# Performance work log

Measured on AMD Instinct MI355X. Metric: run time of the kernel, lower is better.

The kernel has to match this reference:

```python
import jax, jax.numpy as jnp
import numpy as np

B, S, D = 4, 2048, 1024


def setup_inputs() -> dict:
    key = jax.random.key(0)
    k1, k2, k3, k4, k5 = jax.random.split(key, 5)
    x = jax.random.normal(k1, (B, S, D), dtype=jnp.float32)
    mask = jax.random.randint(k2, (B, S), 0, 2).astype(jnp.bool_)
    # glorot-uniform-like init as keras add_weight default
    lim = float(np.sqrt(6.0 / (D + D)))
    q_w = jax.random.uniform(k3, (D, D), minval=-lim, maxval=lim, dtype=jnp.float32)
    k_w = jax.random.uniform(k4, (D, D), minval=-lim, maxval=lim, dtype=jnp.float32)
    v_w = jax.random.uniform(k5, (D, D), minval=-lim, maxval=lim, dtype=jnp.float32)
    return {"x": x, "mask": mask, "q_w": q_w, "k_w": k_w, "v_w": v_w}


def reference(x, mask, q_w, k_w, v_w):
    scale = 1.0 / jnp.sqrt(jnp.asarray(x.shape[-1], dtype=x.dtype))
    q = jnp.einsum('bsi,ij->bsj', x, q_w)
    k = jnp.einsum('bsi,ij->bsj', x, k_w)
    y = jnp.einsum('bsi,bzi->bsz', q, k) * scale  # [B,S,S] scores
    # additive mask applied along the query axis, exactly as the source
    m = (~mask).astype(x.dtype)[:, :, None]
    y = y + m * (-1e9)
    v = jnp.einsum('bsi,ij->bsj', x, v_w)
    p = jax.nn.softmax(y, axis=-1)
    return jnp.einsum('bsz,bzi->bsi', p, v)
```

## Files before the change

kernel.cpp:

```cpp
#include <hip/hip_runtime.h>
#include <hip/hip_bf16.h>

typedef __attribute__((ext_vector_type(8))) short short8;
typedef __attribute__((ext_vector_type(4))) float floatx4;

struct ushort4v { unsigned short x, y, z, w; };

static __device__ __forceinline__ unsigned short f2bf(float f) {
    __hip_bfloat16 h = __float2bfloat16(f);
    return *reinterpret_cast<unsigned short*>(&h);
}

static __device__ __forceinline__ float bf2f(unsigned short u) {
    unsigned int v = ((unsigned int)u) << 16;
    return *reinterpret_cast<float*>(&v);
}

#define ASYNC_COPY16(gsrc, ldst)                                                            \
    __builtin_amdgcn_global_load_lds((const __attribute__((address_space(1))) void*)(gsrc), \
                                     (__attribute__((address_space(3))) void*)(ldst), 16, 0, 0)

static __device__ __forceinline__ void block_barrier() {
    asm volatile("" ::: "memory");
    __builtin_amdgcn_s_barrier();
    asm volatile("" ::: "memory");
}

__global__ void mask_detect(const unsigned char* __restrict__ m, int* __restrict__ flag) {
    __shared__ int s_or;
    if (threadIdx.x == 0) s_or = 0;
    __syncthreads();
    int acc = 0;
    for (int i = threadIdx.x; i < 8192; i += 256)
        if (i & 3) acc |= m[i];
    atomicOr(&s_or, acc);
    __syncthreads();
    if (threadIdx.x == 0) *flag = (s_or != 0) ? 1 : 0;
}

__global__ void mask_expand(const void* __restrict__ m, const int* __restrict__ flag,
                            float* __restrict__ keep, int n) {
    int i = blockIdx.x * 256 + threadIdx.x;
    if (i >= n) return;
    bool on;
    if (*flag)
        on = ((const unsigned char*)m)[i] != 0;
    else
        on = ((const int*)m)[i] != 0;
    keep[i] = on ? 1.0f : 0.0f;
}

__global__ __launch_bounds__(256) void convert_f32_bf16(const float* __restrict__ in,
                                                        unsigned short* __restrict__ out, long n4) {
    long i = (long)blockIdx.x * 256 + threadIdx.x;
    if (i >= n4) return;
    float4 v = ((const float4*)in)[i];
    ushort4v o;
    o.x = f2bf(v.x); o.y = f2bf(v.y); o.z = f2bf(v.z); o.w = f2bf(v.w);
    ((ushort4v*)out)[i] = o;
}

__global__ void transpose_w_kernel(const float* __restrict__ w0, const float* __restrict__ w1,
                                   const float* __restrict__ w2, unsigned short* __restrict__ out) {
    __shared__ float t[32][33];
    const float* w = blockIdx.z == 0 ? w0 : (blockIdx.z == 1 ? w1 : w2);
    unsigned short* o = out + (long)blockIdx.z * 1024 * 1024;
    int c0 = blockIdx.x * 32, r0 = blockIdx.y * 32;
    for (int i = threadIdx.y; i < 32; i += 8)
        t[i][threadIdx.x] = w[(long)(r0 + i) * 1024 + c0 + threadIdx.x];
    __syncthreads();
    for (int i = threadIdx.y; i < 32; i += 8)
        o[(long)(c0 + i) * 1024 + r0 + threadIdx.x] = f2bf(t[threadIdx.x][i]);
}

__global__ void transpose_bf16(const unsigned short* __restrict__ in, unsigned short* __restrict__ out,
                               int rows, int cols, long sIn, long sOut) {
    __shared__ unsigned short t[32][34];
    const unsigned short* ib = in + (long)blockIdx.z * sIn;
    unsigned short* ob = out + (long)blockIdx.z * sOut;
    int c0 = blockIdx.x * 32, r0 = blockIdx.y * 32;
    for (int i = threadIdx.y; i < 32; i += 8)
        t[i][threadIdx.x] = ib[(long)(r0 + i) * cols + c0 + threadIdx.x];
    __syncthreads();
    for (int i = threadIdx.y; i < 32; i += 8)
        ob[(long)(c0 + i) * rows + r0 + threadIdx.x] = t[threadIdx.x][i];
}

template <int EPI>
static __device__ __forceinline__ void gemm8_body(const unsigned short* __restrict__ A,
                                                  const unsigned short* __restrict__ B,
                                                  void* __restrict__ Cv,
                                                  const float* __restrict__ aux,
                                                  int K, int lda, int ldb, int ldc,
                                                  long sA, long sB, long sC, long sAux,
                                                  float scale) {
    constexpr int TILE = (128 + 256) * 32 * 2;
    __shared__ char sm[3 * TILE];

    const int tid = threadIdx.x;
    const int wid = tid >> 6, lane = tid & 63;
    const int wm  = wid >> 2, wn = wid & 3;
    const int fr  = lane & 15, fk = lane >> 4;
    const long m0 = (long)blockIdx.x * 128;
    const long n0 = (long)blockIdx.y * 256;
    const unsigned short* Ab = A + (long)blockIdx.z * sA + m0 * lda;
    const unsigned short* Bb = B + (long)blockIdx.z * sB + n0 * ldb;
    const int NT = K >> 5;

    floatx4 acc[4][4] = {};

    auto stage = [&](int kt, int buf) {
        char* dA = sm + buf * TILE;
        char* dB = dA + 128 * 64;
        const int kb = kt << 5;
        {
            int lam = tid * 16;
            int lg  = lam ^ (((lam >> 7) & 3) << 4);
            ASYNC_COPY16(Ab + (long)(lg >> 6) * lda + kb + ((lg & 63) >> 1), dA + lam);
        }
#pragma unroll
        for (int i = 0; i < 2; i++) {
            int lam = i * 8192 + tid * 16;
            int lg  = lam ^ (((lam >> 7) & 3) << 4);
            ASYNC_COPY16(Bb + (long)(lg >> 6) * ldb + kb + ((lg & 63) >> 1), dB + lam);
        }
    };

    stage(0, 0);
    stage(1, 1);

    int cur = 0;
    for (int t = 0; t < NT; t++) {
        if (t + 1 < NT) asm volatile("s_waitcnt vmcnt(3)" ::: "memory");
        else            asm volatile("s_waitcnt vmcnt(0)" ::: "memory");
        block_barrier();

        const char* bA = sm + cur * TILE;
        const char* bB = bA + 128 * 64;
        short8 af[4], bf[4];
#pragma unroll
        for (int mi = 0; mi < 4; mi++) {
            int row = wm * 64 + mi * 16 + fr;
            int c   = (fk * 16) ^ (((row >> 1) & 3) << 4);
            af[mi] = *(const short8*)(bA + row * 64 + c);
        }
#pragma unroll
        for (int ni = 0; ni < 4; ni++) {
            int row = wn * 64 + ni * 16 + fr;
            int c   = (fk * 16) ^ (((row >> 1) & 3) << 4);
            bf[ni] = *(const short8*)(bB + row * 64 + c);
        }
        if (t + 2 < NT) stage(t + 2, (cur + 2) % 3);

        __builtin_amdgcn_s_setprio(1);
#pragma unroll
        for (int mi = 0; mi < 4; mi++)
#pragma unroll
            for (int ni = 0; ni < 4; ni++)
                acc[mi][ni] = __builtin_amdgcn_mfma_f32_16x16x32_bf16(af[mi], bf[ni], acc[mi][ni], 0, 0, 0);
        __builtin_amdgcn_s_setprio(0);
        cur = (cur == 2) ? 0 : cur + 1;
    }

    const int crow = (lane >> 4) * 4;
    const int ccol = lane & 15;
#pragma unroll
    for (int mi = 0; mi < 4; mi++) {
#pragma unroll
        for (int j = 0; j < 4; j++) {
            long r = m0 + wm * 64 + mi * 16 + crow + j;
            float rowf = 0.0f;
            if (EPI == 1) rowf = scale * aux[(long)blockIdx.z * sAux + r];
            if (EPI == 2) rowf = aux[(long)blockIdx.z * sAux + r];
#pragma unroll
            for (int ni = 0; ni < 4; ni++) {
                long c = n0 + wn * 64 + ni * 16 + ccol;
                float v = acc[mi][ni][j];
                if (EPI == 0) {
                    ((unsigned short*)Cv)[(long)blockIdx.z * sC + r * ldc + c] = f2bf(v);
                } else if (EPI == 1) {
                    ((unsigned short*)Cv)[(long)blockIdx.z * sC + r * ldc + c] = f2bf(__expf(v * rowf));
                } else {
                    ((float*)Cv)[(long)blockIdx.z * sC + r * ldc + c] = v * rowf;
                }
            }
        }
    }
}

__global__ __launch_bounds__(512, 4) void gemm8_qkv(const unsigned short* __restrict__ A,
                                                    const unsigned short* __restrict__ B,
                                                    void* __restrict__ Cv,
                                                    int K, int lda, int ldb, int ldc,
                                                    long sA, long sB, long sC) {
    gemm8_body<0>(A, B, Cv, nullptr, K, lda, ldb, ldc, sA, sB, sC, 0L, 1.0f);
}

__global__ __launch_bounds__(512, 4) void gemm8_scores(const unsigned short* __restrict__ A,
                                                       const unsigned short* __restrict__ B,
                                                       void* __restrict__ Cv,
                                                       const float* __restrict__ keep,
                                                       int K, int lda, int ldb, int ldc,
                                                       long sA, long sB, long sC, long sAux,
                                                       float scale) {
    gemm8_body<1>(A, B, Cv, keep, K, lda, ldb, ldc, sA, sB, sC, sAux, scale);
}

__global__ __launch_bounds__(512, 4) void gemm8_pv(const unsigned short* __restrict__ A,
                                                   const unsigned short* __restrict__ B,
                                                   void* __restrict__ Cv,
                                                   const float* __restrict__ invsum,
                                                   int K, int lda, int ldb, int ldc,
                                                   long sA, long sB, long sC, long sAux) {
    gemm8_body<2>(A, B, Cv, invsum, K, lda, ldb, ldc, sA, sB, sC, sAux, 1.0f);
}

__global__ __launch_bounds__(256) void rowsum_inv(const unsigned short* __restrict__ P,
                                                  float* __restrict__ inv, long strideP) {
    const int tid = threadIdx.x;
    const long row = blockIdx.x;
    short8 v = ((const short8*)(P + row * strideP))[tid];
    float s = 0.0f;
#pragma unroll
    for (int i = 0; i < 8; i++) s += bf2f((unsigned short)v[i]);
#pragma unroll
    for (int i = 1; i < 64; i <<= 1) s += __shfl_xor(s, i);
    __shared__ float ss[4];
    if ((tid & 63) == 0) ss[tid >> 6] = s;
    __syncthreads();
    if (tid == 0) {
        float t = (ss[0] + ss[1]) + (ss[2] + ss[3]);
        inv[row] = 1.0f / t;
    }
}

extern "C" void kernel_launch(void* const* d_in, const int* in_sizes, int n_in,
                              void* d_out, int out_size, void* d_ws, size_t ws_size,
                              hipStream_t stream) {
    const float* x  = (const float*)d_in[0];
    const void*  mask = d_in[1];
    const float* qw = (const float*)d_in[2];
    const float* kw = (const float*)d_in[3];
    const float* vw = (const float*)d_in[4];
    float* out = (float*)d_out;

    constexpr int B = 4, S = 2048, D = 1024;
    constexpr long BS  = (long)B * S;
    constexpr long BSD = BS * D;

    char* w = (char*)d_ws;
    auto alloc = [&](size_t bytes) {
        char* p = w;
        w += (bytes + 255) & ~(size_t)255;
        return p;
    };
    int*            flag    = (int*)alloc(256);
    float*          keep    = (float*)alloc(BS * 4);
    float*          invsum  = (float*)alloc(BS * 4);
    unsigned short* xb      = (unsigned short*)alloc((size_t)BSD * 2);
    unsigned short* wT      = (unsigned short*)alloc((size_t)3 * D * D * 2);
    unsigned short* qkv     = (unsigned short*)alloc((size_t)3 * BSD * 2);
    unsigned short* Qb = qkv;
    unsigned short* Kb = qkv + BSD;
    unsigned short* Vb = qkv + 2 * BSD;
    unsigned short* Vt      = (unsigned short*)alloc((size_t)BSD * 2);

    size_t base_used = (size_t)(w - (char*)d_ws);
    size_t pB = (size_t)B * S * S * 2;
    bool batched = ws_size >= base_used + pB + 1024;

    unsigned short* P;
    if (batched) {
        P = (unsigned short*)alloc(pB);
    } else {
        P = (unsigned short*)alloc((size_t)S * S * 2);
    }

    const float scale = 0.03125f;

    mask_detect<<<1, 256, 0, stream>>>((const unsigned char*)mask, flag);
    mask_expand<<<(int)(BS / 256), 256, 0, stream>>>(mask, flag, keep, (int)BS);
    convert_f32_bf16<<<(int)(BSD / 1024), 256, 0, stream>>>(x, xb, BSD / 4);
    transpose_w_kernel<<<dim3(32, 32, 3), dim3(32, 8), 0, stream>>>(qw, kw, vw, wT);

    gemm8_qkv<<<dim3(64, 4, 3), 512, 0, stream>>>(xb, wT, qkv,
                                                  1024, 1024, 1024, 1024,
                                                  0L, (long)D * D, BSD);

    transpose_bf16<<<dim3(D / 32, S / 32, B), dim3(32, 8), 0, stream>>>(Vb, Vt, S, D,
                                                                        (long)S * D, (long)S * D);

    if (batched) {
        gemm8_scores<<<dim3(16, 8, B), 512, 0, stream>>>(Qb, Kb, P, keep,
                                                         1024, 1024, 1024, 2048,
                                                         (long)S * D, (long)S * D, (long)S * S, (long)S, scale);
        rowsum_inv<<<(int)BS, 256, 0, stream>>>(P, invsum, 2048);
        gemm8_pv<<<dim3(16, 4, B), 512, 0, stream>>>(P, Vt, out, invsum,
                                                     2048, 2048, 2048, 1024,
                                                     (long)S * S, (long)D * S, (long)S * D, (long)S);
    } else {
        for (int b = 0; b < B; b++) {
            gemm8_scores<<<dim3(16, 8, 1), 512, 0, stream>>>(Qb + (long)b * S * D, Kb + (long)b * S * D,
                                                             P, keep + (long)b * S,
                                                             1024, 1024, 1024, 2048,
                                                             0L, 0L, 0L, 0L, scale);
            rowsum_inv<<<S, 256, 0, stream>>>(P, invsum + (long)b * S, 2048);
            gemm8_pv<<<dim3(16, 4, 1), 512, 0, stream>>>(P, Vt + (long)b * D * S, out + (long)b * S * D,
                                                         invsum + (long)b * S,
                                                         2048, 2048, 2048, 1024,
                                                         0L, 0L, 0L, 0L);
        }
    }
}
```

Measured before the change: 178.6 us.

## Use 256x256 tiled GEMM with 4-phase double-buffered pipeline for QKV and scores

Adds a new GEMM body with 256x256 output tiles, 64-wide K steps, XOR-swizzled LDS layout and a double-buffered schedule that splits each K tile into four phases. Each phase issues the async load for the next tile's quarter before running its MFMAs. The QKV projection and score GEMMs move to this kernel, while PV keeps the old 128x256 kernel, now specialised. The larger tiles are meant to raise arithmetic intensity and cut global traffic, at the cost of fewer blocks (lower occupancy, launch bounds of 2) and 128KB of LDS per block.

```diff
diff --git a/kernel.cpp b/kernel.cpp
--- a/kernel.cpp
+++ b/kernel.cpp
@@ -87,13 +87,135 @@
 }
 
 template <int EPI>
-static __device__ __forceinline__ void gemm8_body(const unsigned short* __restrict__ A,
-                                                  const unsigned short* __restrict__ B,
-                                                  void* __restrict__ Cv,
-                                                  const float* __restrict__ aux,
-                                                  int K, int lda, int ldb, int ldc,
-                                                  long sA, long sB, long sC, long sAux,
-                                                  float scale) {
+static __device__ __forceinline__ void gemm256_body(const unsigned short* __restrict__ A,
+                                                    const unsigned short* __restrict__ B,
+                                                    void* __restrict__ Cv,
+                                                    const float* __restrict__ aux,
+                                                    int K, int lda, int ldb, int ldc,
+                                                    long sA, long sB, long sC, long sAux,
+                                                    float scale) {
+    constexpr int BUF = 65536;
+    __shared__ char sm[2 * BUF];
+    const int tid = threadIdx.x;
+    const int wid = tid >> 6, lane = tid & 63;
+    const int wm = wid >> 2, wn = wid & 3;
+    const int fr = lane & 15, fk = lane >> 4;
+    const long m0 = (long)blockIdx.x * 256;
+    const long n0 = (long)blockIdx.y * 256;
+    const unsigned short* Ab = A + (long)blockIdx.z * sA + m0 * lda;
+    const unsigned short* Bb = B + (long)blockIdx.z * sB + n0 * ldb;
+    const int NKT = K >> 6;
+
+    floatx4 acc[8][4] = {};
+
+    auto stage_unit = [&](int kt, int u) {
+        const int isB  = (u == 1 || u == 2) ? 1 : 0;
+        const int half = (u >= 2) ? 1 : 0;
+        char* dst = sm + (kt & 1) * BUF + isB * 32768 + half * 16384;
+        const unsigned short* src = isB ? Bb : Ab;
+        const int ld = isB ? ldb : lda;
+        const int kb = kt << 6;
+#pragma unroll
+        for (int l = 0; l < 2; l++) {
+            int lam = l * 8192 + tid * 16;
+            int lg  = lam ^ (((lam >> 7) & 7) << 4);
+            ASYNC_COPY16(src + (long)(half * 128 + (lg >> 7)) * ld + kb + ((lg & 127) >> 1),
+                         dst + lam);
+        }
+    };
+
+    auto phase = [&](int kt, int ks, int mh, int u, int vm_end) {
+        const char* bA = sm + (kt & 1) * BUF;
+        const char* bB = bA + 32768;
+        const int ca = (ks * 64 + fk * 16) ^ ((fr & 7) << 4);
+        short8 af[4], bf[4];
+#pragma unroll
+        for (int mi = 0; mi < 4; mi++) {
+            int row = mh * 128 + wm * 64 + mi * 16 + fr;
+            af[mi] = *(const short8*)(bA + row * 128 + ca);
+        }
+#pragma unroll
+        for (int ni = 0; ni < 4; ni++) {
+            int row = wn * 64 + ni * 16 + fr;
+            bf[ni] = *(const short8*)(bB + row * 128 + ca);
+        }
+        if (kt + 1 < NKT) stage_unit(kt + 1, u);
+        block_barrier();
+        asm volatile("s_waitcnt lgkmcnt(0)" ::: "memory");
+        __builtin_amdgcn_sched_barrier(0);
+        __builtin_amdgcn_s_setprio(1);
+#pragma unroll
+        for (int mi = 0; mi < 4; mi++)
+#pragma unroll
+            for (int ni = 0; ni < 4; ni++)
+                acc[mh * 4 + mi][ni] =
+                    __builtin_amdgcn_mfma_f32_16x16x32_bf16(af[mi], bf[ni], acc[mh * 4 + mi][ni], 0, 0, 0);
+        __builtin_amdgcn_s_setprio(0);
+        if (vm_end == 2)      asm volatile("s_waitcnt vmcnt(2)" ::: "memory");
+        else if (vm_end == 0) asm volatile("s_waitcnt vmcnt(0)" ::: "memory");
+        block_barrier();
+    };
+
+    stage_unit(0, 0); stage_unit(0, 1); stage_unit(0, 2); stage_unit(0, 3);
+    asm volatile("s_waitcnt vmcnt(2)" ::: "memory");
+    block_barrier();
+
+    for (int kt = 0; kt < NKT; kt++) {
+        const bool more = (kt + 1 < NKT);
+        phase(kt, 0, 0, 0, more ? 2 : 0);
+        phase(kt, 0, 1, 1, -1);
+        phase(kt, 1, 0, 2, -1);
+        phase(kt, 1, 1, 3, more ? 2 : -1);
+    }
+
+    const int crow = (lane >> 4) * 4;
+    const int ccol = lane & 15;
+#pragma unroll
+    for (int a = 0; a < 8; a++) {
+        const int mh = a >> 2, mi = a & 3;
+#pragma unroll
+        for (int j = 0; j < 4; j++) {
+            long r = m0 + mh * 128 + wm * 64 + mi * 16 + crow + j;
+            float rowf = 0.0f;
+            if (EPI == 1) rowf = scale * aux[(long)blockIdx.z * sAux + r];
+#pragma unroll
+            for (int ni = 0; ni < 4; ni++) {
+                long c = n0 + wn * 64 + ni * 16 + ccol;
+                float v = acc[a][ni][j];
+                if (EPI == 0) {
+                    ((unsigned short*)Cv)[(long)blockIdx.z * sC + r * ldc + c] = f2bf(v);
+                } else {
+                    ((unsigned short*)Cv)[(long)blockIdx.z * sC + r * ldc + c] = f2bf(__expf(v * rowf));
+                }
+            }
+        }
+    }
+}
+
+__global__ __launch_bounds__(512, 2) void gemm256_qkv(const unsigned short* __restrict__ A,
+                                                      const unsigned short* __restrict__ B,
+                                                      void* __restrict__ Cv,
+                                                      int K, int lda, int ldb, int ldc,
+                                                      long sA, long sB, long sC) {
+    gemm256_body<0>(A, B, Cv, nullptr, K, lda, ldb, ldc, sA, sB, sC, 0L, 1.0f);
+}
+
+__global__ __launch_bounds__(512, 2) void gemm256_scores(const unsigned short* __restrict__ A,
+                                                         const unsigned short* __restrict__ B,
+                                                         void* __restrict__ Cv,
+                                                         const float* __restrict__ keep,
+                                                         int K, int lda, int ldb, int ldc,
+                                                         long sA, long sB, long sC, long sAux,
+                                                         float scale) {
+    gemm256_body<1>(A, B, Cv, keep, K, lda, ldb, ldc, sA, sB, sC, sAux, scale);
+}
+
+__global__ __launch_bounds__(512, 4) void gemm8_pv(const unsigned short* __restrict__ A,
+                                                   const unsigned short* __restrict__ B,
+                                                   void* __restrict__ Cv,
+                                                   const float* __restrict__ invsum,
+                                                   int K, int lda, int ldb, int ldc,
+                                                   long sA, long sB, long sC, long sAux) {
     constexpr int TILE = (128 + 256) * 32 * 2;
     __shared__ char sm[3 * TILE];
 
@@ -169,50 +291,14 @@
 #pragma unroll
         for (int j = 0; j < 4; j++) {
             long r = m0 + wm * 64 + mi * 16 + crow + j;
-            float rowf = 0.0f;
-            if (EPI == 1) rowf = scale * aux[(long)blockIdx.z * sAux + r];
-            if (EPI == 2) rowf = aux[(long)blockIdx.z * sAux + r];
+            float rowf = invsum[(long)blockIdx.z * sAux + r];
 #pragma unroll
             for (int ni = 0; ni < 4; ni++) {
                 long c = n0 + wn * 64 + ni * 16 + ccol;
-                float v = acc[mi][ni][j];
-                if (EPI == 0) {
-                    ((unsigned short*)Cv)[(long)blockIdx.z * sC + r * ldc + c] = f2bf(v);
-                } else if (EPI == 1) {
-                    ((unsigned short*)Cv)[(long)blockIdx.z * sC + r * ldc + c] = f2bf(__expf(v * rowf));
-                } else {
-                    ((float*)Cv)[(long)blockIdx.z * sC + r * ldc + c] = v * rowf;
-                }
+                ((float*)Cv)[(long)blockIdx.z * sC + r * ldc + c] = acc[mi][ni][j] * rowf;
             }
         }
     }
-}
-
-__global__ __launch_bounds__(512, 4) void gemm8_qkv(const unsigned short* __restrict__ A,
-                                                    const unsigned short* __restrict__ B,
-                                                    void* __restrict__ Cv,
-                                                    int K, int lda, int ldb, int ldc,
-                                                    long sA, long sB, long sC) {
-    gemm8_body<0>(A, B, Cv, nullptr, K, lda, ldb, ldc, sA, sB, sC, 0L, 1.0f);
-}
-
-__global__ __launch_bounds__(512, 4) void gemm8_scores(const unsigned short* __restrict__ A,
-                                                       const unsigned short* __restrict__ B,
-                                                       void* __restrict__ Cv,
-                                                       const float* __restrict__ keep,
-                                                       int K, int lda, int ldb, int ldc,
-                                                       long sA, long sB, long sC, long sAux,
-                                                       float scale) {
-    gemm8_body<1>(A, B, Cv, keep, K, lda, ldb, ldc, sA, sB, sC, sAux, scale);
-}
-
-__global__ __launch_bounds__(512, 4) void gemm8_pv(const unsigned short* __restrict__ A,
-                                                   const unsigned short* __restrict__ B,
-                                                   void* __restrict__ Cv,
-                                                   const float* __restrict__ invsum,
-                                                   int K, int lda, int ldb, int ldc,
-                                                   long sA, long sB, long sC, long sAux) {
-    gemm8_body<2>(A, B, Cv, invsum, K, lda, ldb, ldc, sA, sB, sC, sAux, 1.0f);
 }
 
 __global__ __launch_bounds__(256) void rowsum_inv(const unsigned short* __restrict__ P,
@@ -283,27 +369,27 @@
     convert_f32_bf16<<<(int)(BSD / 1024), 256, 0, stream>>>(x, xb, BSD / 4);
     transpose_w_kernel<<<dim3(32, 32, 3), dim3(32, 8), 0, stream>>>(qw, kw, vw, wT);
 
-    gemm8_qkv<<<dim3(64, 4, 3), 512, 0, stream>>>(xb, wT, qkv,
-                                                  1024, 1024, 1024, 1024,
-                                                  0L, (long)D * D, BSD);
+    gemm256_qkv<<<dim3(32, 4, 3), 512, 0, stream>>>(xb, wT, qkv,
+                                                    1024, 1024, 1024, 1024,
+                                                    0L, (long)D * D, BSD);
 
     transpose_bf16<<<dim3(D / 32, S / 32, B), dim3(32, 8), 0, stream>>>(Vb, Vt, S, D,
                                                                         (long)S * D, (long)S * D);
 
     if (batched) {
-        gemm8_scores<<<dim3(16, 8, B), 512, 0, stream>>>(Qb, Kb, P, keep,
-                                                         1024, 1024, 1024, 2048,
-                                                         (long)S * D, (long)S * D, (long)S * S, (long)S, scale);
+        gemm256_scores<<<dim3(8, 8, B), 512, 0, stream>>>(Qb, Kb, P, keep,
+                                                          1024, 1024, 1024, 2048,
+                                                          (long)S * D, (long)S * D, (long)S * S, (long)S, scale);
         rowsum_inv<<<(int)BS, 256, 0, stream>>>(P, invsum, 2048);
         gemm8_pv<<<dim3(16, 4, B), 512, 0, stream>>>(P, Vt, out, invsum,
                                                      2048, 2048, 2048, 1024,
                                                      (long)S * S, (long)D * S, (long)S * D, (long)S);
     } else {
         for (int b = 0; b < B; b++) {
-            gemm8_scores<<<dim3(16, 8, 1), 512, 0, stream>>>(Qb + (long)b * S * D, Kb + (long)b * S * D,
-                                                             P, keep + (long)b * S,
-                                                             1024, 1024, 1024, 2048,
-                                                             0L, 0L, 0L, 0L, scale);
+            gemm256_scores<<<dim3(8, 8, 1), 512, 0, stream>>>(Qb + (long)b * S * D, Kb + (long)b * S * D,
+                                                              P, keep + (long)b * S,
+                                                              1024, 1024, 1024, 2048,
+                                                              0L, 0L, 0L, 0L, scale);
             rowsum_inv<<<S, 256, 0, stream>>>(P, invsum + (long)b * S, 2048);
             gemm8_pv<<<dim3(16, 4, 1), 512, 0, stream>>>(P, Vt + (long)b * D * S, out + (long)b * S * D,
                                                          invsum + (long)b * S,
```

Result: slower. 194.3 us (+8.8%).

## Fuse V transpose into QKV GEMM epilogue and merge mask kernels

Applied to the files above, without the earlier changes.

The QKV GEMM now writes its V output already transposed. For the V slice it stages the accumulator tile through shared memory and stores it with vectorized writes into the transposed buffer, so the separate transpose_bf16 kernel and its full read and write of V are gone. The mask detect and expand kernels are also merged into one, with every block recomputing the encoding check itself. This saves launches and memory traffic, at the cost of each block redundantly scanning the first 8 KB of the mask and extra LDS work in the epilogue of the V blocks.

```diff
diff --git a/kernel.cpp b/kernel.cpp
--- a/kernel.cpp
+++ b/kernel.cpp
@@ -26,7 +26,8 @@
     asm volatile("" ::: "memory");
 }
 
-__global__ void mask_detect(const unsigned char* __restrict__ m, int* __restrict__ flag) {
+__global__ __launch_bounds__(256) void mask_expand_fused(const unsigned char* __restrict__ m,
+                                                         float* __restrict__ keep, int n) {
     __shared__ int s_or;
     if (threadIdx.x == 0) s_or = 0;
     __syncthreads();
@@ -35,19 +36,12 @@
         if (i & 3) acc |= m[i];
     atomicOr(&s_or, acc);
     __syncthreads();
-    if (threadIdx.x == 0) *flag = (s_or != 0) ? 1 : 0;
-}
-
-__global__ void mask_expand(const void* __restrict__ m, const int* __restrict__ flag,
-                            float* __restrict__ keep, int n) {
+    const bool u8enc = (s_or != 0);
     int i = blockIdx.x * 256 + threadIdx.x;
-    if (i >= n) return;
-    bool on;
-    if (*flag)
-        on = ((const unsigned char*)m)[i] != 0;
-    else
-        on = ((const int*)m)[i] != 0;
-    keep[i] = on ? 1.0f : 0.0f;
+    if (i < n) {
+        bool on = u8enc ? (m[i] != 0) : (((const int*)m)[i] != 0);
+        keep[i] = on ? 1.0f : 0.0f;
+    }
 }
 
 __global__ __launch_bounds__(256) void convert_f32_bf16(const float* __restrict__ in,
@@ -73,23 +67,11 @@
         o[(long)(c0 + i) * 1024 + r0 + threadIdx.x] = f2bf(t[threadIdx.x][i]);
 }
 
-__global__ void transpose_bf16(const unsigned short* __restrict__ in, unsigned short* __restrict__ out,
-                               int rows, int cols, long sIn, long sOut) {
-    __shared__ unsigned short t[32][34];
-    const unsigned short* ib = in + (long)blockIdx.z * sIn;
-    unsigned short* ob = out + (long)blockIdx.z * sOut;
-    int c0 = blockIdx.x * 32, r0 = blockIdx.y * 32;
-    for (int i = threadIdx.y; i < 32; i += 8)
-        t[i][threadIdx.x] = ib[(long)(r0 + i) * cols + c0 + threadIdx.x];
-    __syncthreads();
-    for (int i = threadIdx.y; i < 32; i += 8)
-        ob[(long)(c0 + i) * rows + r0 + threadIdx.x] = t[threadIdx.x][i];
-}
-
 template <int EPI>
 static __device__ __forceinline__ void gemm8_body(const unsigned short* __restrict__ A,
                                                   const unsigned short* __restrict__ B,
                                                   void* __restrict__ Cv,
+                                                  unsigned short* __restrict__ vt,
                                                   const float* __restrict__ aux,
                                                   int K, int lda, int ldb, int ldc,
                                                   long sA, long sB, long sC, long sAux,
@@ -164,6 +146,37 @@
 
     const int crow = (lane >> 4) * 4;
     const int ccol = lane & 15;
+
+    if (EPI == 0 && blockIdx.z == 2) {
+        block_barrier();
+        unsigned short* T = (unsigned short*)sm;
+        constexpr int LDT = 132;
+#pragma unroll
+        for (int mi = 0; mi < 4; mi++)
+#pragma unroll
+            for (int j = 0; j < 4; j++) {
+                int rl = wm * 64 + mi * 16 + crow + j;
+#pragma unroll
+                for (int ni = 0; ni < 4; ni++) {
+                    int cl = wn * 64 + ni * 16 + ccol;
+                    T[cl * LDT + rl] = f2bf(acc[mi][ni][j]);
+                }
+            }
+        block_barrier();
+        const long bb   = m0 >> 11;
+        const long sloc = m0 & 2047;
+        unsigned short* vb = vt + bb * (1024L * 2048) + sloc;
+#pragma unroll
+        for (int p = 0; p < 8; p++) {
+            int chunk = p * 512 + tid;
+            int d  = chunk >> 4;
+            int s0 = (chunk & 15) * 8;
+            short8 v = *(const short8*)&T[d * LDT + s0];
+            *(short8*)(vb + (n0 + d) * 2048 + s0) = v;
+        }
+        return;
+    }
+
 #pragma unroll
     for (int mi = 0; mi < 4; mi++) {
 #pragma unroll
@@ -191,9 +204,10 @@
 __global__ __launch_bounds__(512, 4) void gemm8_qkv(const unsigned short* __restrict__ A,
                                                     const unsigned short* __restrict__ B,
                                                     void* __restrict__ Cv,
+                                                    unsigned short* __restrict__ vt,
                                                     int K, int lda, int ldb, int ldc,
                                                     long sA, long sB, long sC) {
-    gemm8_body<0>(A, B, Cv, nullptr, K, lda, ldb, ldc, sA, sB, sC, 0L, 1.0f);
+    gemm8_body<0>(A, B, Cv, vt, nullptr, K, lda, ldb, ldc, sA, sB, sC, 0L, 1.0f);
 }
 
 __global__ __launch_bounds__(512, 4) void gemm8_scores(const unsigned short* __restrict__ A,
@@ -203,7 +217,7 @@
                                                        int K, int lda, int ldb, int ldc,
                                                        long sA, long sB, long sC, long sAux,
                                                        float scale) {
-    gemm8_body<1>(A, B, Cv, keep, K, lda, ldb, ldc, sA, sB, sC, sAux, scale);
+    gemm8_body<1>(A, B, Cv, nullptr, keep, K, lda, ldb, ldc, sA, sB, sC, sAux, scale);
 }
 
 __global__ __launch_bounds__(512, 4) void gemm8_pv(const unsigned short* __restrict__ A,
@@ -212,7 +226,7 @@
                                                    const float* __restrict__ invsum,
                                                    int K, int lda, int ldb, int ldc,
                                                    long sA, long sB, long sC, long sAux) {
-    gemm8_body<2>(A, B, Cv, invsum, K, lda, ldb, ldc, sA, sB, sC, sAux, 1.0f);
+    gemm8_body<2>(A, B, Cv, nullptr, invsum, K, lda, ldb, ldc, sA, sB, sC, sAux, 1.0f);
 }
 
 __global__ __launch_bounds__(256) void rowsum_inv(const unsigned short* __restrict__ P,
@@ -254,15 +268,13 @@
         w += (bytes + 255) & ~(size_t)255;
         return p;
     };
-    int*            flag    = (int*)alloc(256);
     float*          keep    = (float*)alloc(BS * 4);
     float*          invsum  = (float*)alloc(BS * 4);
     unsigned short* xb      = (unsigned short*)alloc((size_t)BSD * 2);
     unsigned short* wT      = (unsigned short*)alloc((size_t)3 * D * D * 2);
-    unsigned short* qkv     = (unsigned short*)alloc((size_t)3 * BSD * 2);
-    unsigned short* Qb = qkv;
-    unsigned short* Kb = qkv + BSD;
-    unsigned short* Vb = qkv + 2 * BSD;
+    unsigned short* qk      = (unsigned short*)alloc((size_t)2 * BSD * 2);
+    unsigned short* Qb = qk;
+    unsigned short* Kb = qk + BSD;
     unsigned short* Vt      = (unsigned short*)alloc((size_t)BSD * 2);
 
     size_t base_used = (size_t)(w - (char*)d_ws);
@@ -278,17 +290,13 @@
 
     const float scale = 0.03125f;
 
-    mask_detect<<<1, 256, 0, stream>>>((const unsigned char*)mask, flag);
-    mask_expand<<<(int)(BS / 256), 256, 0, stream>>>(mask, flag, keep, (int)BS);
+    mask_expand_fused<<<(int)(BS / 256), 256, 0, stream>>>((const unsigned char*)mask, keep, (int)BS);
     convert_f32_bf16<<<(int)(BSD / 1024), 256, 0, stream>>>(x, xb, BSD / 4);
     transpose_w_kernel<<<dim3(32, 32, 3), dim3(32, 8), 0, stream>>>(qw, kw, vw, wT);
 
-    gemm8_qkv<<<dim3(64, 4, 3), 512, 0, stream>>>(xb, wT, qkv,
+    gemm8_qkv<<<dim3(64, 4, 3), 512, 0, stream>>>(xb, wT, qk, Vt,
                                                   1024, 1024, 1024, 1024,
                                                   0L, (long)D * D, BSD);
-
-    transpose_bf16<<<dim3(D / 32, S / 32, B), dim3(32, 8), 0, stream>>>(Vb, Vt, S, D,
-                                                                        (long)S * D, (long)S * D);
 
     if (batched) {
         gemm8_scores<<<dim3(16, 8, B), 512, 0, stream>>>(Qb, Kb, P, keep,
```

Measured after the change: 171.4 us. -4.1%, faster.
